# Kernel optimization log

Measured on AMD Instinct MI355X. Metric: run time of the kernel, lower is better.

The kernel has to match this reference:

```python
import jax, jax.numpy as jnp
import numpy as np

B, T, D = 4, 2048, 1024
DK, DV = 1024, 1024
BETA1, BETA2 = 1.0, 1.0
EPS = 1e-12  # torch F.normalize eps


def setup_inputs() -> dict:
    key = jax.random.key(0)
    kx, kq, kk, kv, ko = jax.random.split(key, 5)
    def w(k, shape):
        return jax.random.normal(k, shape, dtype=jnp.float32) * (shape[0] ** -0.5)
    return {
        "x": jax.random.normal(kx, (B, T, D), dtype=jnp.float32),
        # Weights stored [in, out]; torch Linear is x @ W.T with W [out, in] -- equivalent math.
        "Wq": w(kq, (D, DK)),
        "Wk": w(kk, (D, DK)),
        "Wv": w(kv, (D, DV)),
        "Wo": w(ko, (DV, D)),
    }


def reference(x, Wq, Wk, Wv, Wo):
    scale = DK ** -0.5
    q = (x @ Wq) * scale                      # [B,T,DK]
    k = x @ Wk
    k = k / jnp.maximum(jnp.linalg.norm(k, axis=-1, keepdims=True), EPS)
    v = x @ Wv                                # [B,T,DV]
    # time-major for scan
    qT = jnp.swapaxes(q, 0, 1)
    kT = jnp.swapaxes(k, 0, 1)
    vT = jnp.swapaxes(v, 0, 1)
    S0 = jnp.zeros((B, DV, DK), dtype=x.dtype)

    def step(S, qkv_t):
        q_t, k_t, v_t = qkv_t                 # each [B, d]
        # S @ (I - b1 k k^T) = S - b1 (S k) k^T   (same math, rank-1 form)
        Sk = jnp.einsum('bvk,bk->bv', S, k_t)
        S = S - BETA1 * Sk[:, :, None] * k_t[:, None, :] \
              + BETA2 * v_t[:, :, None] * k_t[:, None, :]
        o_t = jnp.einsum('bvk,bk->bv', S, q_t)
        return S, o_t

    _, oT = jax.lax.scan(step, S0, (qT, kT, vT))  # oT: [T,B,DV]
    out = jnp.swapaxes(oT, 0, 1) @ Wo             # [B,T,D]
    return out
```

## Files before the change

kernel.cpp:

```cpp
#include <hip/hip_runtime.h>

typedef unsigned short u16;
typedef __attribute__((ext_vector_type(8))) short short8;
typedef __attribute__((ext_vector_type(4))) float floatx4;

#define B_ 4
#define T_ 2048
#define CH 64

__device__ __forceinline__ u16 f2bf(float f) {
  unsigned int x = __float_as_uint(f);
  return (u16)((x + 0x7FFFu + ((x >> 16) & 1u)) >> 16);
}
__device__ __forceinline__ float bf2f(u16 u) {
  union { unsigned int i; float f; } v; v.i = ((unsigned int)u) << 16; return v.f;
}

__global__ __launch_bounds__(256) void xconv_kernel(const float* __restrict__ x,
                                                    u16* __restrict__ Xbf) {
  size_t idx = ((size_t)blockIdx.x * 256 + threadIdx.x) * 4;
  float4 v = *reinterpret_cast<const float4*>(&x[idx]);
  ushort4 o;
  o.x = f2bf(v.x); o.y = f2bf(v.y); o.z = f2bf(v.z); o.w = f2bf(v.w);
  *reinterpret_cast<ushort4*>(&Xbf[idx]) = o;
}

__global__ __launch_bounds__(256) void wtrans_kernel(
    const float* __restrict__ W0, const float* __restrict__ W1,
    const float* __restrict__ W2, const float* __restrict__ W3,
    u16* __restrict__ T0, u16* __restrict__ T1,
    u16* __restrict__ T2, u16* __restrict__ T3)
{
  const int z = blockIdx.z;
  const float* W = (z == 0) ? W0 : (z == 1) ? W1 : (z == 2) ? W2 : W3;
  u16* T = (z == 0) ? T0 : (z == 1) ? T1 : (z == 2) ? T2 : T3;
  const int k0 = blockIdx.x * 64, n0 = blockIdx.y * 64;
  const int tid = threadIdx.x;
  __shared__ float Tile[64][65];
#pragma unroll
  for (int i = 0; i < 4; ++i) {
    int lin = tid + i * 256;
    int r = lin >> 4, c4 = (lin & 15) * 4;
    *reinterpret_cast<float4*>(&Tile[r][c4]) =
        *reinterpret_cast<const float4*>(&W[(size_t)(k0 + r) * 1024 + n0 + c4]);
  }
  __syncthreads();
#pragma unroll
  for (int i = 0; i < 4; ++i) {
    int lin = tid + i * 256;
    int r = lin >> 4, c4 = (lin & 15) * 4;
    ushort4 o;
    o.x = f2bf(Tile[c4 + 0][r]); o.y = f2bf(Tile[c4 + 1][r]);
    o.z = f2bf(Tile[c4 + 2][r]); o.w = f2bf(Tile[c4 + 3][r]);
    *reinterpret_cast<ushort4*>(&T[(size_t)(n0 + r) * 1024 + k0 + c4]) = o;
  }
}

__global__ __launch_bounds__(256) void mgemm_qkv(
    const u16* __restrict__ Xbf,
    const u16* __restrict__ WqT, const u16* __restrict__ WkT, const u16* __restrict__ WvT,
    u16* __restrict__ Qbf, u16* __restrict__ Kbf, u16* __restrict__ Vbf,
    int tg, int lsh)
{
  const int z = blockIdx.z;
  const u16* BT = (z == 0) ? WqT : ((z == 1) ? WkT : WvT);
  u16* O = (z == 0) ? Qbf : ((z == 1) ? Kbf : Vbf);
  const float scale = (z == 0) ? 0.03125f : 1.0f;
  const int r0 = blockIdx.x * 128, c0 = blockIdx.y * 128;
  const int tid = threadIdx.x;
  const int lane = tid & 63, wave = tid >> 6;
  const int quad = lane >> 4, l16 = lane & 15;
  const int wr = (wave >> 1) * 64, wc = (wave & 1) * 64;

  __shared__ u16 As[128][40];
  __shared__ u16 Bs[128][40];

  const int ar = tid >> 1, ac = (tid & 1) * 16;
  const int lr = r0 + ar;
  const int agrow = ((lr >> lsh) << 11) + tg + (lr & ((1 << lsh) - 1));
  const u16* aptr = &Xbf[(size_t)agrow * 1024 + ac];
  const u16* bptr = &BT[(size_t)(c0 + ar) * 1024 + ac];

  floatx4 acc[4][4] = {};
  for (int k0 = 0; k0 < 1024; k0 += 32) {
    float4 av0 = *reinterpret_cast<const float4*>(aptr + k0);
    float4 av1 = *reinterpret_cast<const float4*>(aptr + k0 + 8);
    float4 bv0 = *reinterpret_cast<const float4*>(bptr + k0);
    float4 bv1 = *reinterpret_cast<const float4*>(bptr + k0 + 8);
    __syncthreads();
    *reinterpret_cast<float4*>(&As[ar][ac]) = av0;
    *reinterpret_cast<float4*>(&As[ar][ac + 8]) = av1;
    *reinterpret_cast<float4*>(&Bs[ar][ac]) = bv0;
    *reinterpret_cast<float4*>(&Bs[ar][ac + 8]) = bv1;
    __syncthreads();
    short8 afr[4], bfr[4];
#pragma unroll
    for (int i = 0; i < 4; ++i) {
      afr[i] = *reinterpret_cast<const short8*>(&As[wr + i * 16 + l16][quad * 8]);
      bfr[i] = *reinterpret_cast<const short8*>(&Bs[wc + i * 16 + l16][quad * 8]);
    }
#pragma unroll
    for (int mi = 0; mi < 4; ++mi)
#pragma unroll
      for (int ni = 0; ni < 4; ++ni)
        acc[mi][ni] = __builtin_amdgcn_mfma_f32_16x16x32_bf16(afr[mi], bfr[ni], acc[mi][ni], 0, 0, 0);
  }
#pragma unroll
  for (int mi = 0; mi < 4; ++mi)
#pragma unroll
    for (int reg = 0; reg < 4; ++reg) {
      int row = r0 + wr + mi * 16 + quad * 4 + reg;
#pragma unroll
      for (int ni = 0; ni < 4; ++ni) {
        int col = c0 + wc + ni * 16 + l16;
        O[(size_t)row * 1024 + col] = f2bf(acc[mi][ni][reg] * scale);
      }
    }
}

__global__ __launch_bounds__(256) void mgemm_out(
    const u16* __restrict__ Obf, const u16* __restrict__ WoT,
    float* __restrict__ out, int tg, int lsh)
{
  const int r0 = blockIdx.x * 128, c0 = blockIdx.y * 128;
  const int tid = threadIdx.x;
  const int lane = tid & 63, wave = tid >> 6;
  const int quad = lane >> 4, l16 = lane & 15;
  const int wr = (wave >> 1) * 64, wc = (wave & 1) * 64;

  __shared__ u16 As[128][40];
  __shared__ u16 Bs[128][40];

  const int ar = tid >> 1, ac = (tid & 1) * 16;
  const u16* aptr = &Obf[(size_t)(r0 + ar) * 1024 + ac];
  const u16* bptr = &WoT[(size_t)(c0 + ar) * 1024 + ac];

  floatx4 acc[4][4] = {};
  for (int k0 = 0; k0 < 1024; k0 += 32) {
    float4 av0 = *reinterpret_cast<const float4*>(aptr + k0);
    float4 av1 = *reinterpret_cast<const float4*>(aptr + k0 + 8);
    float4 bv0 = *reinterpret_cast<const float4*>(bptr + k0);
    float4 bv1 = *reinterpret_cast<const float4*>(bptr + k0 + 8);
    __syncthreads();
    *reinterpret_cast<float4*>(&As[ar][ac]) = av0;
    *reinterpret_cast<float4*>(&As[ar][ac + 8]) = av1;
    *reinterpret_cast<float4*>(&Bs[ar][ac]) = bv0;
    *reinterpret_cast<float4*>(&Bs[ar][ac + 8]) = bv1;
    __syncthreads();
    short8 afr[4], bfr[4];
#pragma unroll
    for (int i = 0; i < 4; ++i) {
      afr[i] = *reinterpret_cast<const short8*>(&As[wr + i * 16 + l16][quad * 8]);
      bfr[i] = *reinterpret_cast<const short8*>(&Bs[wc + i * 16 + l16][quad * 8]);
    }
#pragma unroll
    for (int mi = 0; mi < 4; ++mi)
#pragma unroll
      for (int ni = 0; ni < 4; ++ni)
        acc[mi][ni] = __builtin_amdgcn_mfma_f32_16x16x32_bf16(afr[mi], bfr[ni], acc[mi][ni], 0, 0, 0);
  }
#pragma unroll
  for (int mi = 0; mi < 4; ++mi)
#pragma unroll
    for (int reg = 0; reg < 4; ++reg) {
      int lr = r0 + wr + mi * 16 + quad * 4 + reg;
      int grow = ((lr >> lsh) << 11) + tg + (lr & ((1 << lsh) - 1));
#pragma unroll
      for (int ni = 0; ni < 4; ++ni) {
        int col = c0 + wc + ni * 16 + l16;
        out[(size_t)grow * 1024 + col] = acc[mi][ni][reg];
      }
    }
}

__global__ __launch_bounds__(256) void knorm_kernel(u16* __restrict__ Kbf) {
  const int row = blockIdx.x;
  const int tid = threadIdx.x;
  ushort4 v4 = *reinterpret_cast<const ushort4*>(&Kbf[(size_t)row * 1024 + tid * 4]);
  float a = bf2f(v4.x), b = bf2f(v4.y), c = bf2f(v4.z), d = bf2f(v4.w);
  float ss = a * a + b * b + c * c + d * d;
#pragma unroll
  for (int off = 32; off > 0; off >>= 1) ss += __shfl_down(ss, off);
  __shared__ float wsum[4];
  if ((tid & 63) == 0) wsum[tid >> 6] = ss;
  __syncthreads();
  float tot = wsum[0] + wsum[1] + wsum[2] + wsum[3];
  float inv = 1.0f / fmaxf(sqrtf(tot), 1e-12f);
  ushort4 o;
  o.x = f2bf(a * inv); o.y = f2bf(b * inv); o.z = f2bf(c * inv); o.w = f2bf(d * inv);
  *reinterpret_cast<ushort4*>(&Kbf[(size_t)row * 1024 + tid * 4]) = o;
}

__global__ __launch_bounds__(256) void ktrans_kernel(const u16* __restrict__ Kbf,
                                                     u16* __restrict__ KT,
                                                     int tgs) {
  const int t0 = blockIdx.x * 64;
  const int d0 = blockIdx.y * 64;
  const int b = blockIdx.z;
  const int tid = threadIdx.x;
  __shared__ u16 Tile[64][68];
#pragma unroll
  for (int i = 0; i < 4; ++i) {
    int lin = tid + i * 256;
    int r = lin >> 4, c4 = (lin & 15) * 4;
    *reinterpret_cast<ushort4*>(&Tile[r][c4]) =
        *reinterpret_cast<const ushort4*>(&Kbf[(size_t)(b * tgs + t0 + r) * 1024 + d0 + c4]);
  }
  __syncthreads();
#pragma unroll
  for (int i = 0; i < 4; ++i) {
    int lin = tid + i * 256;
    int r = lin >> 4, c4 = (lin & 15) * 4;
    ushort4 o;
    o.x = Tile[c4 + 0][r]; o.y = Tile[c4 + 1][r];
    o.z = Tile[c4 + 2][r]; o.w = Tile[c4 + 3][r];
    *reinterpret_cast<ushort4*>(&KT[((size_t)b * 1024 + d0 + r) * tgs + t0 + c4]) = o;
  }
}

__global__ __launch_bounds__(256) void attn_winv_kernel(
    const u16* __restrict__ Qbf, const u16* __restrict__ Kbf,
    u16* __restrict__ Pb, u16* __restrict__ Wb, int tgs)
{
  const int cc = blockIdx.x;
  const int b = blockIdx.y;
  const int base = b * tgs + cc * CH;
  const int tid = threadIdx.x;
  const int lane = tid & 63;
  const int wave = tid >> 6;
  const int quad = lane >> 4, l16 = lane & 15;
  const int m0 = wave * 16;

  __shared__ float Asm[64][64];
  __shared__ float Wsm[64][65];

  floatx4 accA[4] = {};
  floatx4 accP[4] = {};
  const u16* arowK = &Kbf[(size_t)(base + m0 + l16) * 1024];
  const u16* arowQ = &Qbf[(size_t)(base + m0 + l16) * 1024];
#pragma unroll 4
  for (int kk = 0; kk < 32; ++kk) {
    short8 aK = *reinterpret_cast<const short8*>(&arowK[kk * 32 + quad * 8]);
    short8 aQ = *reinterpret_cast<const short8*>(&arowQ[kk * 32 + quad * 8]);
#pragma unroll
    for (int nt = 0; nt < 4; ++nt) {
      short8 bK = *reinterpret_cast<const short8*>(
          &Kbf[(size_t)(base + nt * 16 + l16) * 1024 + kk * 32 + quad * 8]);
      accA[nt] = __builtin_amdgcn_mfma_f32_16x16x32_bf16(aK, bK, accA[nt], 0, 0, 0);
      accP[nt] = __builtin_amdgcn_mfma_f32_16x16x32_bf16(aQ, bK, accP[nt], 0, 0, 0);
    }
  }
  const size_t pw0 = ((size_t)(cc * B_ + b) * CH) * 64;
#pragma unroll
  for (int nt = 0; nt < 4; ++nt) {
#pragma unroll
    for (int reg = 0; reg < 4; ++reg) {
      int t = m0 + quad * 4 + reg;
      int i = nt * 16 + l16;
      Asm[t][i] = (i < t) ? accA[nt][reg] : 0.0f;
      Pb[pw0 + (size_t)t * 64 + i] = f2bf((i <= t) ? accP[nt][reg] : 0.0f);
    }
  }
  __syncthreads();

  if (tid < 64) {
    const int j = tid;
    for (int t = 0; t < 64; ++t) {
      float s = (t == j) ? 1.0f : 0.0f;
      for (int i = 0; i < t; ++i) s -= Asm[t][i] * Wsm[i][j];
      Wsm[t][j] = s;
    }
    for (int t = 0; t < 64; ++t)
      Wb[pw0 + (size_t)t * 64 + j] = f2bf(Wsm[t][j]);
  }
}

__global__ __launch_bounds__(512) void chain_kernel(
    const u16* __restrict__ Qbf, const u16* __restrict__ Kbf,
    const u16* __restrict__ KT, const u16* __restrict__ Vbf,
    u16* __restrict__ Obf, const u16* __restrict__ Wb, const u16* __restrict__ Pb,
    float* __restrict__ Sglob, int lsh, int cpg, int g, int ngrp)
{
  const int wg = blockIdx.x;
  const int b = wg >> 6;
  const int sl = wg & 63;
  const int c0 = sl * 16;
  const int tgs = 1 << lsh;
  const int tid = threadIdx.x;
  const int lane = tid & 63;
  const int wave = tid >> 6;
  const int quad = lane >> 4, l16 = lane & 15;

  __shared__ float Ssl[16][1028];
  __shared__ u16 Sb[16][1040];
  __shared__ u16 rhsT[16][80];
  __shared__ u16 uT[16][80];

  if (g == 0) {
    for (int idx = tid; idx < 16 * 1024; idx += 512) {
      int r = idx >> 10, d = idx & 1023;
      Ssl[r][d] = 0.0f;
      Sb[r][d] = 0;
    }
  } else {
    for (int idx = tid; idx < 16 * 1024; idx += 512) {
      int r = idx >> 10, d = idx & 1023;
      float v = Sglob[((size_t)b * 1024 + c0 + r) * 1024 + d];
      Ssl[r][d] = v;
      Sb[r][d] = f2bf(v);
    }
  }
  __syncthreads();

  const bool isK = (wave < 4);
  const int mt = isK ? wave : (wave - 4);
  const int m0 = mt * 16;

  for (int cc = 0; cc < cpg; ++cc) {
    const int base = b * tgs + cc * CH;
    const size_t pw0 = ((size_t)(cc * B_ + b) * CH) * 64;

    floatx4 accS = {};
    {
      const u16* arow = (isK ? Kbf : Qbf) + (size_t)(base + m0 + l16) * 1024;
#pragma unroll 8
      for (int kk = 0; kk < 32; ++kk) {
        short8 a = *reinterpret_cast<const short8*>(&arow[kk * 32 + quad * 8]);
        short8 bs = *reinterpret_cast<const short8*>(&Sb[l16][kk * 32 + quad * 8]);
        accS = __builtin_amdgcn_mfma_f32_16x16x32_bf16(a, bs, accS, 0, 0, 0);
      }
    }

    if (isK) {
#pragma unroll
      for (int reg = 0; reg < 4; ++reg) {
        int t = m0 + quad * 4 + reg;
        float v = bf2f(Vbf[(size_t)(base + t) * 1024 + c0 + l16]);
        rhsT[l16][t] = f2bf(v - accS[reg]);
      }
    }
    __syncthreads();

    if (isK) {
      floatx4 uacc = {};
      const u16* wrow = &Wb[pw0 + (size_t)(m0 + l16) * 64];
#pragma unroll
      for (int kk = 0; kk < 2; ++kk) {
        short8 a = *reinterpret_cast<const short8*>(&wrow[kk * 32 + quad * 8]);
        short8 br = *reinterpret_cast<const short8*>(&rhsT[l16][kk * 32 + quad * 8]);
        uacc = __builtin_amdgcn_mfma_f32_16x16x32_bf16(a, br, uacc, 0, 0, 0);
      }
#pragma unroll
      for (int reg = 0; reg < 4; ++reg)
        uT[l16][m0 + quad * 4 + reg] = f2bf(uacc[reg]);
    }
    __syncthreads();

    if (!isK) {
      floatx4 oacc = accS;
      const u16* prow = &Pb[pw0 + (size_t)(m0 + l16) * 64];
#pragma unroll
      for (int kk = 0; kk < 2; ++kk) {
        short8 a = *reinterpret_cast<const short8*>(&prow[kk * 32 + quad * 8]);
        short8 bu = *reinterpret_cast<const short8*>(&uT[l16][kk * 32 + quad * 8]);
        oacc = __builtin_amdgcn_mfma_f32_16x16x32_bf16(a, bu, oacc, 0, 0, 0);
      }
#pragma unroll
      for (int reg = 0; reg < 4; ++reg) {
        int t = m0 + quad * 4 + reg;
        Obf[(size_t)(base + t) * 1024 + c0 + l16] = f2bf(oacc[reg]);
      }
    }

    {
      short8 ua0 = *reinterpret_cast<const short8*>(&uT[l16][quad * 8]);
      short8 ua1 = *reinterpret_cast<const short8*>(&uT[l16][32 + quad * 8]);
      const int d0w = wave * 128;
#pragma unroll
      for (int nt = 0; nt < 8; ++nt) {
        const int dn = d0w + nt * 16;
        const u16* ktrow = &KT[((size_t)b * 1024 + dn + l16) * tgs + cc * CH];
        short8 b0 = *reinterpret_cast<const short8*>(&ktrow[quad * 8]);
        short8 b1 = *reinterpret_cast<const short8*>(&ktrow[32 + quad * 8]);
        floatx4 cf;
        cf[0] = Ssl[quad * 4 + 0][dn + l16];
        cf[1] = Ssl[quad * 4 + 1][dn + l16];
        cf[2] = Ssl[quad * 4 + 2][dn + l16];
        cf[3] = Ssl[quad * 4 + 3][dn + l16];
        cf = __builtin_amdgcn_mfma_f32_16x16x32_bf16(ua0, b0, cf, 0, 0, 0);
        cf = __builtin_amdgcn_mfma_f32_16x16x32_bf16(ua1, b1, cf, 0, 0, 0);
#pragma unroll
        for (int reg = 0; reg < 4; ++reg) {
          Ssl[quad * 4 + reg][dn + l16] = cf[reg];
          Sb[quad * 4 + reg][dn + l16] = f2bf(cf[reg]);
        }
      }
    }
    __syncthreads();
  }

  if (g < ngrp - 1) {
    for (int idx = tid; idx < 16 * 1024; idx += 512) {
      int r = idx >> 10, d = idx & 1023;
      Sglob[((size_t)b * 1024 + c0 + r) * 1024 + d] = Ssl[r][d];
    }
  }
}

extern "C" void kernel_launch(void* const* d_in, const int* in_sizes, int n_in,
                              void* d_out, int out_size, void* d_ws, size_t ws_size,
                              hipStream_t stream) {
  const float* x  = (const float*)d_in[0];
  const float* Wq = (const float*)d_in[1];
  const float* Wk = (const float*)d_in[2];
  const float* Wv = (const float*)d_in[3];
  const float* Wo = (const float*)d_in[4];
  float* out = (float*)d_out;

  int lsh = 8;
  {
    const int cand[4] = {11, 10, 9, 8};
    for (int i = 0; i < 4; ++i) {
      size_t tgs = (size_t)1 << cand[i];
      size_t C = (size_t)B_ * tgs * 1024;
      size_t cpg = tgs / CH;
      size_t need = (size_t)B_ * T_ * 1024 * 2
                  + 4 * ((size_t)1024 * 1024 * 2)
                  + 5 * (C * 2)
                  + 2 * (cpg * B_ * CH * 64 * 2)
                  + (size_t)B_ * 1024 * 1024 * 4
                  + 32768;
      if (need <= ws_size) { lsh = cand[i]; break; }
    }
  }
  const int tgs = 1 << lsh;
  const int cpg = tgs / CH;
  const int ngrp = T_ / tgs;
  const int rows = B_ * tgs;

  char* ws = (char*)d_ws;
  size_t off = 0;
  auto alloc = [&](size_t bytes) -> void* {
    void* p = ws + off;
    off += (bytes + 255) & ~(size_t)255;
    return p;
  };
  u16* Xbf = (u16*)alloc((size_t)B_ * T_ * 1024 * 2);
  u16* WqT = (u16*)alloc((size_t)1024 * 1024 * 2);
  u16* WkT = (u16*)alloc((size_t)1024 * 1024 * 2);
  u16* WvT = (u16*)alloc((size_t)1024 * 1024 * 2);
  u16* WoT = (u16*)alloc((size_t)1024 * 1024 * 2);
  u16* Qbf = (u16*)alloc((size_t)rows * 1024 * 2);
  u16* Kbf = (u16*)alloc((size_t)rows * 1024 * 2);
  u16* Vbf = (u16*)alloc((size_t)rows * 1024 * 2);
  u16* KT  = (u16*)alloc((size_t)rows * 1024 * 2);
  u16* Obf = (u16*)alloc((size_t)rows * 1024 * 2);
  u16* Pb  = (u16*)alloc((size_t)cpg * B_ * CH * 64 * 2);
  u16* Wb  = (u16*)alloc((size_t)cpg * B_ * CH * 64 * 2);
  float* Sglob = (float*)alloc((size_t)B_ * 1024 * 1024 * 4);

  xconv_kernel<<<B_ * T_, 256, 0, stream>>>(x, Xbf);
  wtrans_kernel<<<dim3(16, 16, 4), 256, 0, stream>>>(Wq, Wk, Wv, Wo, WqT, WkT, WvT, WoT);

  for (int g = 0; g < ngrp; ++g) {
    int tg = g * tgs;
    mgemm_qkv<<<dim3(rows / 128, 8, 3), 256, 0, stream>>>(Xbf, WqT, WkT, WvT,
                                                          Qbf, Kbf, Vbf, tg, lsh);
    knorm_kernel<<<rows, 256, 0, stream>>>(Kbf);
    ktrans_kernel<<<dim3(tgs / 64, 16, B_), 256, 0, stream>>>(Kbf, KT, tgs);
    attn_winv_kernel<<<dim3(cpg, B_), 256, 0, stream>>>(Qbf, Kbf, Pb, Wb, tgs);
    chain_kernel<<<256, 512, 0, stream>>>(Qbf, Kbf, KT, Vbf, Obf, Wb, Pb, Sglob,
                                          lsh, cpg, g, ngrp);
    mgemm_out<<<dim3(rows / 128, 8), 256, 0, stream>>>(Obf, WoT, out, tg, lsh);
  }
}
```

Before: 647.6 us.

## Keep fp32 state slice in registers and prefetch chain-kernel operands

```diff
diff --git a/kernel.cpp b/kernel.cpp
--- a/kernel.cpp
+++ b/kernel.cpp
@@ -275,7 +275,7 @@
   }
 }
 
-__global__ __launch_bounds__(512) void chain_kernel(
+__global__ __launch_bounds__(512, 2) void chain_kernel(
     const u16* __restrict__ Qbf, const u16* __restrict__ Kbf,
     const u16* __restrict__ KT, const u16* __restrict__ Vbf,
     u16* __restrict__ Obf, const u16* __restrict__ Wb, const u16* __restrict__ Pb,
@@ -290,66 +290,96 @@
   const int lane = tid & 63;
   const int wave = tid >> 6;
   const int quad = lane >> 4, l16 = lane & 15;
-
-  __shared__ float Ssl[16][1028];
-  __shared__ u16 Sb[16][1040];
-  __shared__ u16 rhsT[16][80];
-  __shared__ u16 uT[16][80];
-
+  const int d0w = wave * 128;
+  const bool isK = (wave < 4);
+  const int m0 = (isK ? wave : (wave - 4)) * 16;
+
+  __shared__ u16 Sb[16][1048];
+  __shared__ u16 rhsT[16][88];
+  __shared__ u16 uT[16][88];
+
+  floatx4 Sreg[8];
   if (g == 0) {
+#pragma unroll
+    for (int nt = 0; nt < 8; ++nt) Sreg[nt] = (floatx4){0.f, 0.f, 0.f, 0.f};
+    for (int idx = tid; idx < 16 * 256; idx += 512) {
+      int r = idx >> 8, d4 = (idx & 255) * 4;
+      ushort4 z4 = {0, 0, 0, 0};
+      *reinterpret_cast<ushort4*>(&Sb[r][d4]) = z4;
+    }
+  } else {
+#pragma unroll
+    for (int nt = 0; nt < 8; ++nt)
+#pragma unroll
+      for (int reg = 0; reg < 4; ++reg)
+        Sreg[nt][reg] = Sglob[((size_t)b * 1024 + c0 + quad * 4 + reg) * 1024 +
+                              d0w + nt * 16 + l16];
     for (int idx = tid; idx < 16 * 1024; idx += 512) {
       int r = idx >> 10, d = idx & 1023;
-      Ssl[r][d] = 0.0f;
-      Sb[r][d] = 0;
-    }
-  } else {
-    for (int idx = tid; idx < 16 * 1024; idx += 512) {
-      int r = idx >> 10, d = idx & 1023;
-      float v = Sglob[((size_t)b * 1024 + c0 + r) * 1024 + d];
-      Ssl[r][d] = v;
-      Sb[r][d] = f2bf(v);
+      Sb[r][d] = f2bf(Sglob[((size_t)b * 1024 + c0 + r) * 1024 + d]);
     }
   }
   __syncthreads();
-
-  const bool isK = (wave < 4);
-  const int mt = isK ? wave : (wave - 4);
-  const int m0 = mt * 16;
 
   for (int cc = 0; cc < cpg; ++cc) {
     const int base = b * tgs + cc * CH;
     const size_t pw0 = ((size_t)(cc * B_ + b) * CH) * 64;
 
-    floatx4 accS = {};
+    float vv[4];
+    if (isK) {
+#pragma unroll
+      for (int reg = 0; reg < 4; ++reg)
+        vv[reg] = bf2f(Vbf[(size_t)(base + m0 + quad * 4 + reg) * 1024 + c0 + l16]);
+    }
+    short8 wpf0, wpf1;
+    {
+      const u16* row = (isK ? Wb : Pb) + pw0 + (size_t)(m0 + l16) * 64;
+      wpf0 = *reinterpret_cast<const short8*>(row + quad * 8);
+      wpf1 = *reinterpret_cast<const short8*>(row + 32 + quad * 8);
+    }
+    short8 ktf[8][2];
+#pragma unroll
+    for (int nt = 0; nt < 8; ++nt) {
+      const u16* ktrow = &KT[((size_t)b * 1024 + d0w + nt * 16 + l16) * tgs + cc * CH];
+      ktf[nt][0] = *reinterpret_cast<const short8*>(ktrow + quad * 8);
+      ktf[nt][1] = *reinterpret_cast<const short8*>(ktrow + 32 + quad * 8);
+    }
+
+    floatx4 ac0 = {}, ac1 = {}, ac2 = {}, ac3 = {};
     {
       const u16* arow = (isK ? Kbf : Qbf) + (size_t)(base + m0 + l16) * 1024;
-#pragma unroll 8
-      for (int kk = 0; kk < 32; ++kk) {
-        short8 a = *reinterpret_cast<const short8*>(&arow[kk * 32 + quad * 8]);
-        short8 bs = *reinterpret_cast<const short8*>(&Sb[l16][kk * 32 + quad * 8]);
-        accS = __builtin_amdgcn_mfma_f32_16x16x32_bf16(a, bs, accS, 0, 0, 0);
+#pragma unroll
+      for (int kk8 = 0; kk8 < 8; ++kk8) {
+        const int kb = kk8 * 4;
+        short8 A0 = *reinterpret_cast<const short8*>(&arow[(kb + 0) * 32 + quad * 8]);
+        short8 A1 = *reinterpret_cast<const short8*>(&arow[(kb + 1) * 32 + quad * 8]);
+        short8 A2 = *reinterpret_cast<const short8*>(&arow[(kb + 2) * 32 + quad * 8]);
+        short8 A3 = *reinterpret_cast<const short8*>(&arow[(kb + 3) * 32 + quad * 8]);
+        short8 B0 = *reinterpret_cast<const short8*>(&Sb[l16][(kb + 0) * 32 + quad * 8]);
+        short8 B1 = *reinterpret_cast<const short8*>(&Sb[l16][(kb + 1) * 32 + quad * 8]);
+        short8 B2 = *reinterpret_cast<const short8*>(&Sb[l16][(kb + 2) * 32 + quad * 8]);
+        short8 B3 = *reinterpret_cast<const short8*>(&Sb[l16][(kb + 3) * 32 + quad * 8]);
+        ac0 = __builtin_amdgcn_mfma_f32_16x16x32_bf16(A0, B0, ac0, 0, 0, 0);
+        ac1 = __builtin_amdgcn_mfma_f32_16x16x32_bf16(A1, B1, ac1, 0, 0, 0);
+        ac2 = __builtin_amdgcn_mfma_f32_16x16x32_bf16(A2, B2, ac2, 0, 0, 0);
+        ac3 = __builtin_amdgcn_mfma_f32_16x16x32_bf16(A3, B3, ac3, 0, 0, 0);
       }
     }
+    floatx4 accS = (ac0 + ac1) + (ac2 + ac3);
 
     if (isK) {
 #pragma unroll
-      for (int reg = 0; reg < 4; ++reg) {
-        int t = m0 + quad * 4 + reg;
-        float v = bf2f(Vbf[(size_t)(base + t) * 1024 + c0 + l16]);
-        rhsT[l16][t] = f2bf(v - accS[reg]);
-      }
+      for (int reg = 0; reg < 4; ++reg)
+        rhsT[l16][m0 + quad * 4 + reg] = f2bf(vv[reg] - accS[reg]);
     }
     __syncthreads();
 
     if (isK) {
       floatx4 uacc = {};
-      const u16* wrow = &Wb[pw0 + (size_t)(m0 + l16) * 64];
-#pragma unroll
-      for (int kk = 0; kk < 2; ++kk) {
-        short8 a = *reinterpret_cast<const short8*>(&wrow[kk * 32 + quad * 8]);
-        short8 br = *reinterpret_cast<const short8*>(&rhsT[l16][kk * 32 + quad * 8]);
-        uacc = __builtin_amdgcn_mfma_f32_16x16x32_bf16(a, br, uacc, 0, 0, 0);
-      }
+      short8 br0 = *reinterpret_cast<const short8*>(&rhsT[l16][quad * 8]);
+      short8 br1 = *reinterpret_cast<const short8*>(&rhsT[l16][32 + quad * 8]);
+      uacc = __builtin_amdgcn_mfma_f32_16x16x32_bf16(wpf0, br0, uacc, 0, 0, 0);
+      uacc = __builtin_amdgcn_mfma_f32_16x16x32_bf16(wpf1, br1, uacc, 0, 0, 0);
 #pragma unroll
       for (int reg = 0; reg < 4; ++reg)
         uT[l16][m0 + quad * 4 + reg] = f2bf(uacc[reg]);
@@ -358,13 +388,10 @@
 
     if (!isK) {
       floatx4 oacc = accS;
-      const u16* prow = &Pb[pw0 + (size_t)(m0 + l16) * 64];
-#pragma unroll
-      for (int kk = 0; kk < 2; ++kk) {
-        short8 a = *reinterpret_cast<const short8*>(&prow[kk * 32 + quad * 8]);
-        short8 bu = *reinterpret_cast<const short8*>(&uT[l16][kk * 32 + quad * 8]);
-        oacc = __builtin_amdgcn_mfma_f32_16x16x32_bf16(a, bu, oacc, 0, 0, 0);
-      }
+      short8 bu0 = *reinterpret_cast<const short8*>(&uT[l16][quad * 8]);
+      short8 bu1 = *reinterpret_cast<const short8*>(&uT[l16][32 + quad * 8]);
+      oacc = __builtin_amdgcn_mfma_f32_16x16x32_bf16(wpf0, bu0, oacc, 0, 0, 0);
+      oacc = __builtin_amdgcn_mfma_f32_16x16x32_bf16(wpf1, bu1, oacc, 0, 0, 0);
 #pragma unroll
       for (int reg = 0; reg < 4; ++reg) {
         int t = m0 + quad * 4 + reg;
@@ -375,35 +402,28 @@
     {
       short8 ua0 = *reinterpret_cast<const short8*>(&uT[l16][quad * 8]);
       short8 ua1 = *reinterpret_cast<const short8*>(&uT[l16][32 + quad * 8]);
-      const int d0w = wave * 128;
 #pragma unroll
       for (int nt = 0; nt < 8; ++nt) {
+        floatx4 cf = Sreg[nt];
+        cf = __builtin_amdgcn_mfma_f32_16x16x32_bf16(ua0, ktf[nt][0], cf, 0, 0, 0);
+        cf = __builtin_amdgcn_mfma_f32_16x16x32_bf16(ua1, ktf[nt][1], cf, 0, 0, 0);
+        Sreg[nt] = cf;
         const int dn = d0w + nt * 16;
-        const u16* ktrow = &KT[((size_t)b * 1024 + dn + l16) * tgs + cc * CH];
-        short8 b0 = *reinterpret_cast<const short8*>(&ktrow[quad * 8]);
-        short8 b1 = *reinterpret_cast<const short8*>(&ktrow[32 + quad * 8]);
-        floatx4 cf;
-        cf[0] = Ssl[quad * 4 + 0][dn + l16];
-        cf[1] = Ssl[quad * 4 + 1][dn + l16];
-        cf[2] = Ssl[quad * 4 + 2][dn + l16];
-        cf[3] = Ssl[quad * 4 + 3][dn + l16];
-        cf = __builtin_amdgcn_mfma_f32_16x16x32_bf16(ua0, b0, cf, 0, 0, 0);
-        cf = __builtin_amdgcn_mfma_f32_16x16x32_bf16(ua1, b1, cf, 0, 0, 0);
-#pragma unroll
-        for (int reg = 0; reg < 4; ++reg) {
-          Ssl[quad * 4 + reg][dn + l16] = cf[reg];
+#pragma unroll
+        for (int reg = 0; reg < 4; ++reg)
           Sb[quad * 4 + reg][dn + l16] = f2bf(cf[reg]);
-        }
       }
     }
     __syncthreads();
   }
 
   if (g < ngrp - 1) {
-    for (int idx = tid; idx < 16 * 1024; idx += 512) {
-      int r = idx >> 10, d = idx & 1023;
-      Sglob[((size_t)b * 1024 + c0 + r) * 1024 + d] = Ssl[r][d];
-    }
+#pragma unroll
+    for (int nt = 0; nt < 8; ++nt)
+#pragma unroll
+      for (int reg = 0; reg < 4; ++reg)
+        Sglob[((size_t)b * 1024 + c0 + quad * 4 + reg) * 1024 + d0w + nt * 16 + l16] =
+            Sreg[nt][reg];
   }
 }
 
```

Measured after the change: 636.9 us. No clear change (-1.6%).
